# Optimization experiments

Hardware: AMD Instinct MI355X
Metric: run time of the kernel (lower is better)

Reference implementation:

```python
import jax, jax.numpy as jnp
import numpy as np

B, L, DM, H = 2, 2048, 1024, 16
D = DM // H  # head_dim = key_dim = 64


def setup_inputs() -> dict:
    key = jax.random.key(0)
    ks = jax.random.split(key, 6)
    w = 0.02
    return {
        "x": jax.random.normal(ks[0], (B, L, DM), dtype=jnp.float32),
        "wq_attn": jax.random.normal(ks[1], (DM, H * D), dtype=jnp.float32) * w,
        "wk_attn": jax.random.normal(ks[2], (DM, H * D), dtype=jnp.float32) * w,
        "wq_rel": jax.random.normal(ks[3], (DM, H * D), dtype=jnp.float32) * w,
        "wk_rel": jax.random.normal(ks[4], (DM, H * D), dtype=jnp.float32) * w,
        "wo": jax.random.normal(ks[5], (H * D, H * D), dtype=jnp.float32) * w,
    }


def reference(x, wq_attn, wk_attn, wq_rel, wk_rel, wo):
    b, l, dm = x.shape
    # projections -> (B, L, H, D); MHA so n_kv_heads == n_heads, no repeat_kv
    q = (x @ wq_attn).reshape(b, l, H, D)
    k = (x @ wk_attn).reshape(b, l, H, D)
    qr = (x @ wq_rel).reshape(b, l, H, D)
    kr = (x @ wk_rel).reshape(b, l, H, D)

    scale = D ** -0.5  # SDPA default: 1/sqrt(query key_dim)
    scores = jnp.einsum("blhd,bmhd->bhlm", q, k) * scale  # (B, H, L, L)
    causal = jnp.tril(jnp.ones((l, l), dtype=bool))
    scores = jnp.where(causal, scores, -jnp.inf)
    attn = jax.nn.softmax(scores, axis=-1)

    # attend over relational keys, then Hadamard with relational queries
    attended_kr = jnp.einsum("bhlm,bmhd->blhd", attn, kr)  # (B, L, H, D)
    attended_relations = qr * attended_kr                    # (B, L, H, D)

    out = attended_relations.reshape(b, l, H * D) @ wo       # (B, L, d_model)
    return out
```

## Files before the change

kernel.cpp:

```cpp
#include <hip/hip_runtime.h>
#include <stdint.h>


typedef __attribute__((ext_vector_type(4))) float floatx4;
typedef __attribute__((ext_vector_type(8))) short shortx8;
typedef __attribute__((ext_vector_type(4))) short shortx4;

__device__ __forceinline__ unsigned short f2bf(float f) {
    unsigned u = __float_as_uint(f);
    u += 0x7fffu + ((u >> 16) & 1u);
    return (unsigned short)(u >> 16);
}
__device__ __forceinline__ float bf2f(unsigned short s) {
    return __uint_as_float(((unsigned)s) << 16);
}
__device__ __forceinline__ float exp2fast(float x) {
#if __has_builtin(__builtin_amdgcn_exp2f)
    return __builtin_amdgcn_exp2f(x);
#else
    return __expf(x * 0.69314718056f);
#endif
}
__device__ __forceinline__ unsigned pkbf(float e0, float e1) {
    return __builtin_amdgcn_perm(__float_as_uint(e1), __float_as_uint(e0), 0x07060302u);
}
__device__ __forceinline__ floatx4 mfma16(shortx4 a, shortx4 b, floatx4 c) {
#if __has_builtin(__builtin_amdgcn_mfma_f32_16x16x16bf16_1k)
    return __builtin_amdgcn_mfma_f32_16x16x16bf16_1k(a, b, c, 0, 0, 0);
#else
    shortx8 a8 = {a[0], a[1], a[2], a[3], 0, 0, 0, 0};
    shortx8 b8 = {b[0], b[1], b[2], b[3], 0, 0, 0, 0};
    return __builtin_amdgcn_mfma_f32_16x16x32_bf16(a8, b8, c, 0, 0, 0);
#endif
}
__device__ __forceinline__ void gll16(const void* g, void* l) {
    __builtin_amdgcn_global_load_lds(
        (const __attribute__((address_space(1))) unsigned int*)g,
        (__attribute__((address_space(3))) unsigned int*)l, 16, 0, 0);
}

__global__ void k_cvt_x(const float* __restrict__ x, unsigned short* __restrict__ xb) {
    int i = (blockIdx.x * 256 + threadIdx.x) * 4;
    float4 v = *(const float4*)(x + i);
    ushort4 o;
    o.x = f2bf(v.x); o.y = f2bf(v.y); o.z = f2bf(v.z); o.w = f2bf(v.w);
    *(ushort4*)(xb + i) = o;
}

__global__ __launch_bounds__(256) void k_cvt_w5(const float* __restrict__ wq,
                                                const float* __restrict__ wk,
                                                const float* __restrict__ wqr,
                                                const float* __restrict__ wkr,
                                                const float* __restrict__ wo,
                                                unsigned short* __restrict__ wcatT,
                                                unsigned short* __restrict__ wotT) {
    __shared__ unsigned short Tl[64 * 65];
    const int t = threadIdx.x;
    const int kt = blockIdx.x * 64, nt = blockIdx.y * 64;
    const int z = blockIdx.z;
    const float* W = (z == 0) ? wq : (z == 1) ? wk : (z == 2) ? wqr : (z == 3) ? wkr : wo;
    unsigned short* outT = (z < 4) ? (wcatT + (size_t)z * 1024 * 1024) : wotT;
    const float scale = (z == 0) ? 0.18033688f : 1.0f;
    {
        const int kl = t >> 3, nc = (t & 7) * 8;
        const float* src = W + (size_t)(kt + kl) * 1024 + nt + nc;
        float a[8], b[8];
        *(float4*)(a)     = *(const float4*)(src);
        *(float4*)(a + 4) = *(const float4*)(src + 4);
        *(float4*)(b)     = *(const float4*)(src + 32 * 1024);
        *(float4*)(b + 4) = *(const float4*)(src + 32 * 1024 + 4);
#pragma unroll
        for (int i = 0; i < 8; ++i) {
            Tl[kl * 65 + nc + i]        = f2bf(a[i] * scale);
            Tl[(kl + 32) * 65 + nc + i] = f2bf(b[i] * scale);
        }
    }
    __syncthreads();
    {
        const int n = t >> 2, kc = (t & 3) * 16;
        shortx8 o0, o1;
#pragma unroll
        for (int i = 0; i < 8; ++i) {
            o0[i] = (short)Tl[(kc + i) * 65 + n];
            o1[i] = (short)Tl[(kc + 8 + i) * 65 + n];
        }
        unsigned short* dst = outT + (size_t)(nt + n) * 1024 + kt + kc;
        *(shortx8*)(dst)     = o0;
        *(shortx8*)(dst + 8) = o1;
    }
}

__global__ __launch_bounds__(256) void k_trans(const unsigned short* __restrict__ qcat,
                                               unsigned short* __restrict__ krT) {
    __shared__ unsigned short Tl[64 * 65];
    const int t = threadIdx.x;
    const int mt = blockIdx.x * 64;
    const int bh = blockIdx.y;
    const int b = bh >> 4, h = bh & 15;
    {
        const int ml = t >> 3, dc = (t & 7) * 8;
        const unsigned short* src =
            qcat + ((size_t)b * 2048 + mt + ml) * 4096 + 3072 + h * 64 + dc;
        shortx8 v0 = *(const shortx8*)(src);
        shortx8 v1 = *(const shortx8*)(src + (size_t)32 * 4096);
#pragma unroll
        for (int i = 0; i < 8; ++i) {
            Tl[ml * 65 + dc + i]        = (unsigned short)v0[i];
            Tl[(ml + 32) * 65 + dc + i] = (unsigned short)v1[i];
        }
    }
    __syncthreads();
    {
        const int d = t >> 2, mc = (t & 3) * 16;
        shortx8 o0, o1;
#pragma unroll
        for (int i = 0; i < 8; ++i) {
            o0[i] = (short)Tl[(mc + i) * 65 + d];
            o1[i] = (short)Tl[(mc + 8 + i) * 65 + d];
        }
        unsigned short* dst = krT + ((size_t)bh * 64 + d) * 2048 + mt + mc;
        *(shortx8*)(dst)     = o0;
        *(shortx8*)(dst + 8) = o1;
    }
}

__global__ __launch_bounds__(256) void k_gemm_bt(const unsigned short* __restrict__ A,
                                                 const unsigned short* __restrict__ Bt,
                                                 unsigned short* __restrict__ C,
                                                 int N, int K) {
    __shared__ alignas(16) unsigned short As[2][128 * 32];
    __shared__ alignas(16) unsigned short Bs[2][128 * 32];
    const int t = threadIdx.x;
    const int lane = t & 63, wv = t >> 6;
    const int ln = lane & 15, quad = lane >> 4;
    const int wm = wv >> 1, wn = wv & 1;
    const int bm = blockIdx.y * 128, bn = blockIdx.x * 128;

    floatx4 acc[4][4] = {};

    const int srow = t >> 2;
    const int sc = (t & 3) ^ ((srow >> 1) & 3);
    const unsigned short* ga0 = A + (size_t)(bm + srow) * K + sc * 8;
    const unsigned short* ga1 = ga0 + (size_t)64 * K;
    const unsigned short* gb0 = Bt + (size_t)(bn + srow) * K + sc * 8;
    const unsigned short* gb1 = gb0 + (size_t)64 * K;

    gll16(ga0, &As[0][wv * 512]);
    gll16(ga1, &As[0][2048 + wv * 512]);
    gll16(gb0, &Bs[0][wv * 512]);
    gll16(gb1, &Bs[0][2048 + wv * 512]);

    const int sw = (ln >> 1) & 3;
    int cur = 0;
    for (int k0 = 0; k0 < K; k0 += 32, cur ^= 1) {
        __syncthreads();
        const int nk = k0 + 32;
        if (nk < K) {
            gll16(ga0 + nk, &As[cur ^ 1][wv * 512]);
            gll16(ga1 + nk, &As[cur ^ 1][2048 + wv * 512]);
            gll16(gb0 + nk, &Bs[cur ^ 1][wv * 512]);
            gll16(gb1 + nk, &Bs[cur ^ 1][2048 + wv * 512]);
        }
        shortx8 af[4], bfr[4];
#pragma unroll
        for (int i = 0; i < 4; ++i)
            af[i] = *(const shortx8*)(&As[cur][(wm * 64 + i * 16 + ln) * 32 + ((quad ^ sw) * 8)]);
#pragma unroll
        for (int j = 0; j < 4; ++j)
            bfr[j] = *(const shortx8*)(&Bs[cur][(wn * 64 + j * 16 + ln) * 32 + ((quad ^ sw) * 8)]);
#pragma unroll
        for (int i = 0; i < 4; ++i)
#pragma unroll
            for (int j = 0; j < 4; ++j)
                acc[i][j] = __builtin_amdgcn_mfma_f32_16x16x32_bf16(af[i], bfr[j], acc[i][j], 0, 0, 0);
    }

#pragma unroll
    for (int i = 0; i < 4; ++i)
#pragma unroll
        for (int j = 0; j < 4; ++j)
#pragma unroll
            for (int r = 0; r < 4; ++r) {
                int row = bm + wm * 64 + i * 16 + quad * 4 + r;
                int col = bn + wn * 64 + j * 16 + ln;
                C[(size_t)row * N + col] = f2bf(acc[i][j][r]);
            }
}

__global__ __launch_bounds__(256) void k_gemm_n64(const unsigned short* __restrict__ A,
                                                  const unsigned short* __restrict__ Bt,
                                                  float* __restrict__ C,
                                                  int N, int K) {
    __shared__ alignas(16) unsigned short As[2][128 * 32];
    __shared__ alignas(16) unsigned short Bs[2][64 * 32];
    const int t = threadIdx.x;
    const int lane = t & 63, wv = t >> 6;
    const int ln = lane & 15, quad = lane >> 4;
    const int bm = blockIdx.y * 128, bn = blockIdx.x * 64;

    floatx4 acc[2][4] = {};

    const int srow = t >> 2;
    const int sc = (t & 3) ^ ((srow >> 1) & 3);
    const unsigned short* ga0 = A + (size_t)(bm + srow) * K + sc * 8;
    const unsigned short* ga1 = ga0 + (size_t)64 * K;
    const unsigned short* gb0 = Bt + (size_t)(bn + srow) * K + sc * 8;

    gll16(ga0, &As[0][wv * 512]);
    gll16(ga1, &As[0][2048 + wv * 512]);
    gll16(gb0, &Bs[0][wv * 512]);

    const int sw = (ln >> 1) & 3;
    int cur = 0;
    for (int k0 = 0; k0 < K; k0 += 32, cur ^= 1) {
        __syncthreads();
        const int nk = k0 + 32;
        if (nk < K) {
            gll16(ga0 + nk, &As[cur ^ 1][wv * 512]);
            gll16(ga1 + nk, &As[cur ^ 1][2048 + wv * 512]);
            gll16(gb0 + nk, &Bs[cur ^ 1][wv * 512]);
        }
        shortx8 af[2], bfr[4];
#pragma unroll
        for (int i = 0; i < 2; ++i)
            af[i] = *(const shortx8*)(&As[cur][(wv * 32 + i * 16 + ln) * 32 + ((quad ^ sw) * 8)]);
#pragma unroll
        for (int j = 0; j < 4; ++j)
            bfr[j] = *(const shortx8*)(&Bs[cur][(j * 16 + ln) * 32 + ((quad ^ sw) * 8)]);
#pragma unroll
        for (int i = 0; i < 2; ++i)
#pragma unroll
            for (int j = 0; j < 4; ++j)
                acc[i][j] = __builtin_amdgcn_mfma_f32_16x16x32_bf16(af[i], bfr[j], acc[i][j], 0, 0, 0);
    }

#pragma unroll
    for (int i = 0; i < 2; ++i)
#pragma unroll
        for (int j = 0; j < 4; ++j)
#pragma unroll
            for (int r = 0; r < 4; ++r) {
                int row = bm + wv * 32 + i * 16 + quad * 4 + r;
                int col = bn + j * 16 + ln;
                C[(size_t)row * N + col] = acc[i][j][r];
            }
}

__global__ __launch_bounds__(256, 2) void k_attn(const unsigned short* __restrict__ qcat,
                                                 const unsigned short* __restrict__ krT,
                                                 unsigned short* __restrict__ ar) {
    __shared__ alignas(16) unsigned short Kl[2][64 * 64];
    __shared__ alignas(16) unsigned short Rl[2][64 * 64];
    __shared__ float Ls[4][4][16];

    const int t = threadIdx.x;
    const int lane = t & 63, w = t >> 6;
    const int ln = lane & 15, quad = lane >> 4;
    const int flat = blockIdx.x;
    const int bh = (flat & 7) * 4 + ((flat >> 3) & 3);
    const int qts = flat >> 5;
    const int qt = (qts & 1) ? 31 - (qts >> 1) : (qts >> 1);
    const int b = bh >> 4, h = bh & 15;
    const int l0 = qt * 64;
    const size_t baserow = (size_t)b * 2048;

    shortx8 aq[4][2];
#pragma unroll
    for (int qc = 0; qc < 4; ++qc) {
        const unsigned short* qp =
            qcat + (baserow + l0 + qc * 16 + ln) * 4096 + h * 64 + quad * 8;
        aq[qc][0] = *(const shortx8*)(qp);
        aq[qc][1] = *(const shortx8*)(qp + 32);
    }

    floatx4 acc_o[4][4] = {};
    float lsum[4] = {0.f, 0.f, 0.f, 0.f};

    const int srow = t >> 3;
    const int sc = (t & 7) ^ (srow & 7);
    const unsigned short* gK = qcat + (baserow + srow) * 4096 + 1024 + h * 64 + sc * 8;
    const unsigned short* gR = krT + ((size_t)bh * 64 + srow) * 2048 + sc * 8;

    auto stage = [&](int kt, int buf) {
        gll16(gK + (size_t)(kt * 64) * 4096,      &Kl[buf][w * 512]);
        gll16(gK + (size_t)(kt * 64 + 32) * 4096, &Kl[buf][2048 + w * 512]);
        gll16(gR + kt * 64,                       &Rl[buf][w * 512]);
        gll16(gR + (size_t)32 * 2048 + kt * 64,   &Rl[buf][2048 + w * 512]);
    };

    stage(0, 0);
    const int swz = ln & 7;
    const int krow = (w * 16 + ln) * 64;
    const int cmw = w * 2 + (quad >> 1);
    int cur = 0;
    for (int kt = 0; kt <= qt; ++kt, cur ^= 1) {
        __syncthreads();
        if (kt < qt) stage(kt + 1, cur ^ 1);
        const unsigned short* Kc = Kl[cur];
        const unsigned short* Rc = Rl[cur];
        const bool diag = (kt == qt);

        shortx8 kf0 = *(const shortx8*)(Kc + krow + ((quad ^ swz) * 8));
        shortx8 kf1 = *(const shortx8*)(Kc + krow + (((4 + quad) ^ swz) * 8));
        shortx4 krf[4];
#pragma unroll
        for (int jd = 0; jd < 4; ++jd)
            krf[jd] = *(const shortx4*)(Rc + (jd * 16 + ln) * 64 +
                                        ((cmw ^ swz) * 8) + (quad & 1) * 4);

        const int keyb = kt * 64 + w * 16 + quad * 4;
        shortx4 pk[4];
#pragma unroll
        for (int qc = 0; qc < 4; ++qc) {
            floatx4 z = {0.f, 0.f, 0.f, 0.f};
            z = __builtin_amdgcn_mfma_f32_16x16x32_bf16(kf0, aq[qc][0], z, 0, 0, 0);
            z = __builtin_amdgcn_mfma_f32_16x16x32_bf16(kf1, aq[qc][1], z, 0, 0, 0);
            float e0 = exp2fast(z[0]);
            float e1 = exp2fast(z[1]);
            float e2 = exp2fast(z[2]);
            float e3 = exp2fast(z[3]);
            if (diag) {
                const int q = l0 + qc * 16 + ln;
                e0 = (keyb + 0 > q) ? 0.f : e0;
                e1 = (keyb + 1 > q) ? 0.f : e1;
                e2 = (keyb + 2 > q) ? 0.f : e2;
                e3 = (keyb + 3 > q) ? 0.f : e3;
            }
            lsum[qc] += (e0 + e1) + (e2 + e3);
            struct U2 { unsigned a, b; } u{pkbf(e0, e1), pkbf(e2, e3)};
            pk[qc] = __builtin_bit_cast(shortx4, u);
        }

#pragma unroll
        for (int qc = 0; qc < 4; ++qc)
#pragma unroll
            for (int jd = 0; jd < 4; ++jd)
                acc_o[qc][jd] = mfma16(krf[jd], pk[qc], acc_o[qc][jd]);
    }

#pragma unroll
    for (int qc = 0; qc < 4; ++qc) {
        float s = lsum[qc];
        s += __shfl_xor(s, 16);
        s += __shfl_xor(s, 32);
        lsum[qc] = s;
    }
    if (lane < 16) {
#pragma unroll
        for (int qc = 0; qc < 4; ++qc) Ls[w][qc][lane] = lsum[qc];
    }

    __syncthreads();
    float* redA = (float*)&Kl[0][0];
    float* redB = (float*)&Rl[0][0];
    if (w >= 2) {
        float* dst = (w == 2) ? redA : redB;
#pragma unroll
        for (int qc = 0; qc < 4; ++qc)
#pragma unroll
            for (int jd = 0; jd < 4; ++jd)
                *(floatx4*)(dst + ((qc * 4 + jd) * 64 + lane) * 4) = acc_o[qc][jd];
    }
    __syncthreads();
    if (w < 2) {
        const float* src = (w == 0) ? redA : redB;
#pragma unroll
        for (int qc = 0; qc < 4; ++qc)
#pragma unroll
            for (int jd = 0; jd < 4; ++jd)
                acc_o[qc][jd] += *(const floatx4*)(src + ((qc * 4 + jd) * 64 + lane) * 4);
    }
    __syncthreads();
    if (w == 1) {
#pragma unroll
        for (int qc = 0; qc < 4; ++qc)
#pragma unroll
            for (int jd = 0; jd < 4; ++jd)
                *(floatx4*)(redA + ((qc * 4 + jd) * 64 + lane) * 4) = acc_o[qc][jd];
    }
    __syncthreads();
    if (w == 0) {
        float inv[4];
#pragma unroll
        for (int qc = 0; qc < 4; ++qc)
            inv[qc] = 1.0f / (Ls[0][qc][ln] + Ls[1][qc][ln] + Ls[2][qc][ln] + Ls[3][qc][ln]);
#pragma unroll
        for (int qc = 0; qc < 4; ++qc) {
            const int q = l0 + qc * 16 + ln;
            const unsigned short* qr = qcat + (baserow + q) * 4096 + 2048 + h * 64;
            unsigned short* arow = ar + (baserow + q) * 1024 + h * 64;
#pragma unroll
            for (int jd = 0; jd < 4; ++jd) {
                floatx4 a = acc_o[qc][jd];
                a += *(const floatx4*)(redA + ((qc * 4 + jd) * 64 + lane) * 4);
                const int d0 = jd * 16 + quad * 4;
                shortx4 qv = *(const shortx4*)(qr + d0);
                shortx4 o;
#pragma unroll
                for (int r = 0; r < 4; ++r)
                    o[r] = (short)f2bf(a[r] * inv[qc] * bf2f((unsigned short)qv[r]));
                *(shortx4*)(arow + d0) = o;
            }
        }
    }
}

extern "C" void kernel_launch(void* const* d_in, const int* in_sizes, int n_in,
                              void* d_out, int out_size, void* d_ws, size_t ws_size,
                              hipStream_t stream) {
    const float* x   = (const float*)d_in[0];
    const float* wq  = (const float*)d_in[1];
    const float* wk  = (const float*)d_in[2];
    const float* wqr = (const float*)d_in[3];
    const float* wkr = (const float*)d_in[4];
    const float* wo  = (const float*)d_in[5];
    float* out = (float*)d_out;

    unsigned short* xb    = (unsigned short*)d_ws;
    unsigned short* wcatT = xb + (size_t)4096 * 1024;
    unsigned short* qcat  = wcatT + (size_t)4096 * 1024;
    unsigned short* wotT  = qcat + (size_t)4096 * 4096;
    unsigned short* krT   = wcatT;
    unsigned short* arb   = xb;

    k_cvt_x<<<4096, 256, 0, stream>>>(x, xb);
    k_cvt_w5<<<dim3(16, 16, 5), 256, 0, stream>>>(wq, wk, wqr, wkr, wo, wcatT, wotT);
    k_gemm_bt<<<dim3(32, 32), 256, 0, stream>>>(xb, wcatT, qcat, 4096, 1024);
    k_trans<<<dim3(32, 32), 256, 0, stream>>>(qcat, krT);
    k_attn<<<1024, 256, 0, stream>>>(qcat, krT, arb);
    k_gemm_n64<<<dim3(16, 32), 256, 0, stream>>>(arb, wotT, out, 1024, 1024);
}
```

Baseline: 200.3 us.

## Use 256x256-tile projection GEMM with 4-stage async load pipeline and XCD-aware mapping

```diff
diff --git a/kernel.cpp b/kernel.cpp
--- a/kernel.cpp
+++ b/kernel.cpp
@@ -124,64 +124,80 @@
     }
 }
 
-__global__ __launch_bounds__(256) void k_gemm_bt(const unsigned short* __restrict__ A,
-                                                 const unsigned short* __restrict__ Bt,
-                                                 unsigned short* __restrict__ C,
-                                                 int N, int K) {
-    __shared__ alignas(16) unsigned short As[2][128 * 32];
-    __shared__ alignas(16) unsigned short Bs[2][128 * 32];
+__global__ __launch_bounds__(512, 1) void k_gemm_bt256(const unsigned short* __restrict__ A,
+                                                       const unsigned short* __restrict__ Bt,
+                                                       unsigned short* __restrict__ C,
+                                                       int N, int K) {
+    __shared__ alignas(16) unsigned short As[4][256 * 32];
+    __shared__ alignas(16) unsigned short Bs[4][256 * 32];
     const int t = threadIdx.x;
-    const int lane = t & 63, wv = t >> 6;
+    const int lane = t & 63, w = t >> 6;
     const int ln = lane & 15, quad = lane >> 4;
-    const int wm = wv >> 1, wn = wv & 1;
-    const int bm = blockIdx.y * 128, bn = blockIdx.x * 128;
-
-    floatx4 acc[4][4] = {};
+    const int wm = w >> 2, wn = w & 3;
+    const int flat = blockIdx.x;
+    const int xcd = flat & 7, idx = flat >> 3;
+    const int bm = ((xcd >> 1) * 4 + (idx >> 3)) * 256;
+    const int bn = ((xcd & 1) * 8 + (idx & 7)) * 256;
+
+    floatx4 acc[8][4] = {};
 
     const int srow = t >> 2;
     const int sc = (t & 3) ^ ((srow >> 1) & 3);
-    const unsigned short* ga0 = A + (size_t)(bm + srow) * K + sc * 8;
-    const unsigned short* ga1 = ga0 + (size_t)64 * K;
-    const unsigned short* gb0 = Bt + (size_t)(bn + srow) * K + sc * 8;
-    const unsigned short* gb1 = gb0 + (size_t)64 * K;
-
-    gll16(ga0, &As[0][wv * 512]);
-    gll16(ga1, &As[0][2048 + wv * 512]);
-    gll16(gb0, &Bs[0][wv * 512]);
-    gll16(gb1, &Bs[0][2048 + wv * 512]);
+    const unsigned short* gA = A + (size_t)(bm + srow) * K + sc * 8;
+    const unsigned short* gB = Bt + (size_t)(bn + srow) * K + sc * 8;
+    const int w16 = w * 16;
+
+    auto stage = [&](int kt, int buf) {
+        const unsigned short* a = gA + (size_t)kt * 32;
+        const unsigned short* b = gB + (size_t)kt * 32;
+        gll16(a,                    &As[buf][w16 * 32]);
+        gll16(a + (size_t)128 * K,  &As[buf][(128 + w16) * 32]);
+        gll16(b,                    &Bs[buf][w16 * 32]);
+        gll16(b + (size_t)128 * K,  &Bs[buf][(128 + w16) * 32]);
+    };
+
+    const int NT = K >> 5;
+    stage(0, 0); stage(1, 1); stage(2, 2);
 
     const int sw = (ln >> 1) & 3;
-    int cur = 0;
-    for (int k0 = 0; k0 < K; k0 += 32, cur ^= 1) {
-        __syncthreads();
-        const int nk = k0 + 32;
-        if (nk < K) {
-            gll16(ga0 + nk, &As[cur ^ 1][wv * 512]);
-            gll16(ga1 + nk, &As[cur ^ 1][2048 + wv * 512]);
-            gll16(gb0 + nk, &Bs[cur ^ 1][wv * 512]);
-            gll16(gb1 + nk, &Bs[cur ^ 1][2048 + wv * 512]);
-        }
-        shortx8 af[4], bfr[4];
-#pragma unroll
-        for (int i = 0; i < 4; ++i)
-            af[i] = *(const shortx8*)(&As[cur][(wm * 64 + i * 16 + ln) * 32 + ((quad ^ sw) * 8)]);
+    for (int t0 = 0; t0 < NT; ++t0) {
+        asm volatile("" ::: "memory");
+        __builtin_amdgcn_s_barrier();
+        asm volatile("" ::: "memory");
+        if (t0 + 3 < NT) {
+            stage(t0 + 3, (t0 + 3) & 3);
+            asm volatile("s_waitcnt vmcnt(12)" ::: "memory");
+        } else if (t0 + 2 < NT) {
+            asm volatile("s_waitcnt vmcnt(8)" ::: "memory");
+        } else if (t0 + 1 < NT) {
+            asm volatile("s_waitcnt vmcnt(4)" ::: "memory");
+        } else {
+            asm volatile("s_waitcnt vmcnt(0)" ::: "memory");
+        }
+        __builtin_amdgcn_s_barrier();
+        asm volatile("" ::: "memory");
+        const unsigned short* Ab = As[t0 & 3];
+        const unsigned short* Bb = Bs[t0 & 3];
+        shortx8 bfr[4];
 #pragma unroll
         for (int j = 0; j < 4; ++j)
-            bfr[j] = *(const shortx8*)(&Bs[cur][(wn * 64 + j * 16 + ln) * 32 + ((quad ^ sw) * 8)]);
-#pragma unroll
-        for (int i = 0; i < 4; ++i)
+            bfr[j] = *(const shortx8*)(Bb + (wn * 64 + j * 16 + ln) * 32 + ((quad ^ sw) * 8));
+#pragma unroll
+        for (int i = 0; i < 8; ++i) {
+            shortx8 af = *(const shortx8*)(Ab + (wm * 128 + i * 16 + ln) * 32 + ((quad ^ sw) * 8));
 #pragma unroll
             for (int j = 0; j < 4; ++j)
-                acc[i][j] = __builtin_amdgcn_mfma_f32_16x16x32_bf16(af[i], bfr[j], acc[i][j], 0, 0, 0);
-    }
-
-#pragma unroll
-    for (int i = 0; i < 4; ++i)
+                acc[i][j] = __builtin_amdgcn_mfma_f32_16x16x32_bf16(af, bfr[j], acc[i][j], 0, 0, 0);
+        }
+    }
+
+#pragma unroll
+    for (int i = 0; i < 8; ++i)
 #pragma unroll
         for (int j = 0; j < 4; ++j)
 #pragma unroll
             for (int r = 0; r < 4; ++r) {
-                int row = bm + wm * 64 + i * 16 + quad * 4 + r;
+                int row = bm + wm * 128 + i * 16 + quad * 4 + r;
                 int col = bn + wn * 64 + j * 16 + ln;
                 C[(size_t)row * N + col] = f2bf(acc[i][j][r]);
             }
@@ -191,8 +207,8 @@
                                                   const unsigned short* __restrict__ Bt,
                                                   float* __restrict__ C,
                                                   int N, int K) {
-    __shared__ alignas(16) unsigned short As[2][128 * 32];
-    __shared__ alignas(16) unsigned short Bs[2][64 * 32];
+    __shared__ alignas(16) unsigned short As[4][128 * 32];
+    __shared__ alignas(16) unsigned short Bs[4][64 * 32];
     const int t = threadIdx.x;
     const int lane = t & 63, wv = t >> 6;
     const int ln = lane & 15, quad = lane >> 4;
@@ -202,31 +218,45 @@
 
     const int srow = t >> 2;
     const int sc = (t & 3) ^ ((srow >> 1) & 3);
-    const unsigned short* ga0 = A + (size_t)(bm + srow) * K + sc * 8;
-    const unsigned short* ga1 = ga0 + (size_t)64 * K;
-    const unsigned short* gb0 = Bt + (size_t)(bn + srow) * K + sc * 8;
-
-    gll16(ga0, &As[0][wv * 512]);
-    gll16(ga1, &As[0][2048 + wv * 512]);
-    gll16(gb0, &Bs[0][wv * 512]);
+    const unsigned short* gA = A + (size_t)(bm + srow) * K + sc * 8;
+    const unsigned short* gB = Bt + (size_t)(bn + srow) * K + sc * 8;
+
+    auto stage = [&](int kt, int buf) {
+        const unsigned short* a = gA + (size_t)kt * 32;
+        gll16(a,                   &As[buf][wv * 512]);
+        gll16(a + (size_t)64 * K,  &As[buf][2048 + wv * 512]);
+        gll16(gB + (size_t)kt * 32, &Bs[buf][wv * 512]);
+    };
+
+    const int NT = K >> 5;
+    stage(0, 0); stage(1, 1); stage(2, 2);
 
     const int sw = (ln >> 1) & 3;
-    int cur = 0;
-    for (int k0 = 0; k0 < K; k0 += 32, cur ^= 1) {
-        __syncthreads();
-        const int nk = k0 + 32;
-        if (nk < K) {
-            gll16(ga0 + nk, &As[cur ^ 1][wv * 512]);
-            gll16(ga1 + nk, &As[cur ^ 1][2048 + wv * 512]);
-            gll16(gb0 + nk, &Bs[cur ^ 1][wv * 512]);
-        }
+    for (int t0 = 0; t0 < NT; ++t0) {
+        asm volatile("" ::: "memory");
+        __builtin_amdgcn_s_barrier();
+        asm volatile("" ::: "memory");
+        if (t0 + 3 < NT) {
+            stage(t0 + 3, (t0 + 3) & 3);
+            asm volatile("s_waitcnt vmcnt(9)" ::: "memory");
+        } else if (t0 + 2 < NT) {
+            asm volatile("s_waitcnt vmcnt(6)" ::: "memory");
+        } else if (t0 + 1 < NT) {
+            asm volatile("s_waitcnt vmcnt(3)" ::: "memory");
+        } else {
+            asm volatile("s_waitcnt vmcnt(0)" ::: "memory");
+        }
+        __builtin_amdgcn_s_barrier();
+        asm volatile("" ::: "memory");
+        const unsigned short* Ab = As[t0 & 3];
+        const unsigned short* Bb = Bs[t0 & 3];
         shortx8 af[2], bfr[4];
 #pragma unroll
         for (int i = 0; i < 2; ++i)
-            af[i] = *(const shortx8*)(&As[cur][(wv * 32 + i * 16 + ln) * 32 + ((quad ^ sw) * 8)]);
+            af[i] = *(const shortx8*)(Ab + (wv * 32 + i * 16 + ln) * 32 + ((quad ^ sw) * 8));
 #pragma unroll
         for (int j = 0; j < 4; ++j)
-            bfr[j] = *(const shortx8*)(&Bs[cur][(j * 16 + ln) * 32 + ((quad ^ sw) * 8)]);
+            bfr[j] = *(const shortx8*)(Bb + (j * 16 + ln) * 32 + ((quad ^ sw) * 8));
 #pragma unroll
         for (int i = 0; i < 2; ++i)
 #pragma unroll
@@ -425,7 +455,7 @@
 
     k_cvt_x<<<4096, 256, 0, stream>>>(x, xb);
     k_cvt_w5<<<dim3(16, 16, 5), 256, 0, stream>>>(wq, wk, wqr, wkr, wo, wcatT, wotT);
-    k_gemm_bt<<<dim3(32, 32), 256, 0, stream>>>(xb, wcatT, qcat, 4096, 1024);
+    k_gemm_bt256<<<256, 512, 0, stream>>>(xb, wcatT, qcat, 4096, 1024);
     k_trans<<<dim3(32, 32), 256, 0, stream>>>(qcat, krT);
     k_attn<<<1024, 256, 0, stream>>>(qcat, krT, arb);
     k_gemm_n64<<<dim3(16, 32), 256, 0, stream>>>(arb, wotT, out, 1024, 1024);
```

After: 201.0 us. About the same (+0.4%).
